# Kernel optimization log

Hardware: AMD Instinct MI355X
Metric: run time of the kernel (lower is better)

The kernel has to match this reference:

```python
import jax, jax.numpy as jnp
import numpy as np

# Structure constants (layered DAG form of the deepire proof trace)
M, D, R = 2, 128, 8          # ensemble size, embed dim, #inference rules
N0, L, K = 8192, 32, 4096    # init nodes, levels, deriv nodes per level
N_THAX, N_SINE = 1000, 32
N_TOTAL = N0 + L * K
POS_WEIGHT_EXTRA = 1.0


def setup_inputs() -> dict:
    key = jax.random.key(0)
    ks = jax.random.split(key, 8)
    rng = np.random.default_rng(0)
    # --- DAG structure (int, constant) ---
    thax_ids = jnp.asarray(rng.integers(0, N_THAX, N0), jnp.int32)
    sine_ids = jnp.asarray(rng.integers(0, N_SINE, N0), jnp.int32)
    # parents of level-l nodes come only from nodes created before level l
    parents = np.stack([rng.integers(0, N0 + l * K, (K, 2)) for l in range(L)])
    parents = jnp.asarray(parents.astype(np.int32))
    rule_ids = jnp.asarray(rng.integers(0, R, (L, K)), jnp.int32)
    sel = rng.random(N_TOTAL) < 0.1
    pos_cnt = jnp.asarray(np.where(sel, rng.integers(1, 20, N_TOTAL), 0), jnp.float32)
    neg_cnt = jnp.asarray(np.where(sel, rng.integers(0, 20, N_TOTAL), 0), jnp.float32)
    # --- learned params (per ensemble member) ---
    def p(k, shape, scale):
        return (scale * jax.random.normal(k, shape, jnp.float32))
    return dict(
        thax_ids=thax_ids, sine_ids=sine_ids, parents=parents, rule_ids=rule_ids,
        pos_cnt=pos_cnt, neg_cnt=neg_cnt,
        thax_table=p(ks[0], (M, N_THAX, D), 1.0),
        sine_w=p(ks[1], (M, D), 0.1),
        sine_b=p(ks[2], (M, D), 0.1),
        W1=p(ks[3], (M, R, 2 * D, D), (2 * D) ** -0.5),
        b1=jnp.zeros((M, R, D), jnp.float32),
        W2=p(ks[4], (M, R, D, D), D ** -0.5),
        b2=jnp.zeros((M, R, D), jnp.float32),
        w_eval=p(ks[5], (M, D), D ** -0.5),
        b_eval=jnp.zeros((M,), jnp.float32),
    )


def _forward(thax_ids, sine_ids, parents, rule_ids, pos_cnt, neg_cnt,
             thax_table, sine_w, sine_b, W1, b1, W2, b2, w_eval, b_eval):
    # --- init nodes: embedding lookup + sine embellishment ---
    emb = jnp.take(thax_table, thax_ids, axis=1)                  # [M, N0, D]
    s = sine_ids.astype(jnp.float32)[None, :, None]               # [1, N0, 1]
    emb = emb * jax.nn.sigmoid(s * sine_w[:, None, :] + sine_b[:, None, :])
    store = jnp.zeros((N_TOTAL, M, D), jnp.float32)
    store = store.at[:N0].set(jnp.transpose(emb, (1, 0, 2)))      # [N, M, D]

    offsets = N0 + K * jnp.arange(L, dtype=jnp.int32)

    def level(store, xs):
        par, rid, off = xs                                        # [K,2], [K], []
        pe = store[par]                                           # [K, 2, M, D]
        x = jnp.concatenate([pe[:, 0], pe[:, 1]], axis=-1)        # [K, M, 2D]
        # per-rule 2-layer MLP on concatenated parents (CatAndNonLinearBinary)
        h = jax.nn.relu(jnp.einsum('kmd,mrde->kmre', x, W1) + b1[None])
        h = jnp.einsum('kmre,mref->kmrf', h, W2) + b2[None]       # [K, M, R, D]
        new = jnp.take_along_axis(h, rid[:, None, None, None], axis=2)[:, :, 0]
        store = jax.lax.dynamic_update_slice(store, new, (off, 0, 0))
        return store, None

    store, _ = jax.lax.scan(level, store, (parents, rule_ids, offsets))

    # --- evaluation / loss on selected nodes ---
    vals = jnp.einsum('nmd,md->nm', store, w_eval) + b_eval       # [N, M] logits
    cnt = pos_cnt + neg_cnt
    mask = (cnt > 0).astype(jnp.float32)                          # [N]
    gold = jnp.where(cnt > 0, pos_cnt / jnp.maximum(cnt, 1.0), 0.0)
    tot_pos, tot_neg = jnp.sum(pos_cnt), jnp.sum(neg_cnt)
    pw = jnp.where(tot_pos > 0, POS_WEIGHT_EXTRA * tot_neg / jnp.maximum(tot_pos, 1.0), 1.0)
    # BCEWithLogits with pos_weight, stable form
    bce = pw * gold[:, None] * jax.nn.softplus(-vals) \
        + (1.0 - gold)[:, None] * jax.nn.softplus(vals)           # [N, M]
    loss = jnp.sum((mask * cnt)[:, None] * bce, axis=0)           # [M]
    posOK = jnp.sum(mask[:, None] * (vals >= 0) * pos_cnt[:, None], axis=0)
    negOK = jnp.sum(mask[:, None] * (vals < 0) * neg_cnt[:, None], axis=0)
    return loss, posOK, negOK


def reference(thax_ids, sine_ids, parents, rule_ids, pos_cnt, neg_cnt,
              thax_table, sine_w, sine_b, W1, b1, W2, b2, w_eval, b_eval):
    return _forward(thax_ids, sine_ids, parents, rule_ids, pos_cnt, neg_cnt,
                    thax_table, sine_w, sine_b, W1, b1, W2, b2, w_eval, b_eval)
```

## Files before the change

### kernel.cpp

```cpp
#include <hip/hip_runtime.h>
#include <cstdint>
#include <cstddef>

#define MM 2
#define DD 128
#define RR 8
#define NN0 8192
#define LLV 32
#define KK 4096
#define NTHAX 1000
#define NTOT (NN0 + LLV*KK)
#define NB 16
#define CHN16 264
#define EBLK 2048
#define TBLK 64

typedef short bf16x8 __attribute__((ext_vector_type(8)));
typedef float f32x4  __attribute__((ext_vector_type(4)));

__device__ __forceinline__ unsigned short f2bf(float f){
  union { float f; uint32_t u; } x; x.f = f;
  uint32_t u = x.u + 0x7FFFu + ((x.u >> 16) & 1u);
  return (unsigned short)(u >> 16);
}

__global__ void prep_kernel(const int* __restrict__ rule_ids,
                            int* __restrict__ chunk_nodes,
                            int* __restrict__ chunk_rule,
                            int* __restrict__ nchunks)
{
  const int l = blockIdx.x, t = threadIdx.x;
  __shared__ int cnt[RR], start[RR], fill[RR];
  if (t < RR){ cnt[t] = 0; fill[t] = 0; }
  __syncthreads();
  for (int k = t; k < KK; k += blockDim.x) atomicAdd(&cnt[rule_ids[l*KK + k]], 1);
  __syncthreads();
  if (t == 0){
    int s = 0;
    for (int r = 0; r < RR; ++r){
      start[r] = s;
      int pad = (cnt[r] + NB - 1)/NB*NB;
      for (int c = s/NB; c < (s+pad)/NB; ++c) chunk_rule[l*CHN16 + c] = r;
      s += pad;
    }
    nchunks[l] = s/NB;
  }
  __syncthreads();
  for (int i = t; i < CHN16*NB; i += blockDim.x) chunk_nodes[l*CHN16*NB + i] = -1;
  __syncthreads();
  for (int k = t; k < KK; k += blockDim.x){
    int r = rule_ids[l*KK + k];
    int p = start[r] + atomicAdd(&fill[r], 1);
    chunk_nodes[l*CHN16*NB + p] = k;
  }
}

__global__ void convw_kernel(const float* __restrict__ W, unsigned short* __restrict__ Wt, int K)
{
  int idx = blockIdx.x*blockDim.x + threadIdx.x;
  if (idx >= MM*RR*K*DD) return;
  int e = idx & 127;
  int k = (idx >> 7) % K;
  int mr = idx / (K*DD);
  float v = W[((size_t)mr*K + k)*DD + e];
  int kb = k >> 3, j = k & 7;
  Wt[((size_t)mr*(K >> 3) + kb)*DD*8 + e*8 + j] = f2bf(v);
}

__global__ void init_kernel(const int* __restrict__ thax_ids, const int* __restrict__ sine_ids,
                            const float* __restrict__ thax_table,
                            const float* __restrict__ sine_w, const float* __restrict__ sine_b,
                            float* __restrict__ store)
{
  int idx = blockIdx.x*blockDim.x + threadIdx.x;
  if (idx >= NN0*MM*DD) return;
  int i = idx >> 8;
  int md = idx & 255;
  int m = md >> 7, d = md & 127;
  float emb = thax_table[((size_t)m*NTHAX + thax_ids[i])*DD + d];
  float s = (float)sine_ids[i];
  float z = s*sine_w[m*DD + d] + sine_b[m*DD + d];
  float sig = 1.f/(1.f + expf(-z));
  store[idx] = emb*sig;
}

__global__ void totals_kernel(const float* __restrict__ pos, const float* __restrict__ neg,
                              float* __restrict__ pt)
{
  __shared__ float ts[4][2];
  const int t = threadIdx.x, lane = t & 63;
  float sp = 0.f, sn = 0.f;
  for (int n = blockIdx.x*blockDim.x + t; n < NTOT; n += gridDim.x*blockDim.x){
    sp += pos[n]; sn += neg[n];
  }
  #pragma unroll
  for (int s = 1; s < 64; s <<= 1){ sp += __shfl_xor(sp, s, 64); sn += __shfl_xor(sn, s, 64); }
  if (lane == 0){ ts[t>>6][0] = sp; ts[t>>6][1] = sn; }
  __syncthreads();
  if (t < 2) pt[t*TBLK + blockIdx.x] = ts[0][t] + ts[1][t] + ts[2][t] + ts[3][t];
}

__global__ __launch_bounds__(256, 2) void level_kernel(
    float* __restrict__ store,
    const int* __restrict__ parents,
    const int* __restrict__ chunk_nodes,
    const int* __restrict__ chunk_rule,
    const int* __restrict__ nchunks,
    const unsigned short* __restrict__ W1t, const float* __restrict__ b1,
    const unsigned short* __restrict__ W2t, const float* __restrict__ b2,
    int level)
{
  const int c = blockIdx.x;
  if (c >= nchunks[level]) return;
  const int m = blockIdx.y;
  const int r = chunk_rule[level*CHN16 + c];

  __shared__ __align__(16) unsigned short Xs[16*256];
  __shared__ __align__(16) unsigned short Hs[16*128];
  __shared__ int nd[NB];
  __shared__ int par[NB][2];

  const int t  = threadIdx.x;
  const int w  = t >> 6;
  const int l  = t & 63;
  const int lr = l & 15;
  const int lg = l >> 4;

  if (t < NB){
    int node = chunk_nodes[(level*CHN16 + c)*NB + t];
    nd[t] = node;
    const int* parL = parents + (size_t)level*KK*2;
    int p0 = 0, p1 = 0;
    if (node >= 0){ p0 = parL[node*2]; p1 = parL[node*2 + 1]; }
    par[t][0] = p0; par[t][1] = p1;
  }
  __syncthreads();

  #pragma unroll
  for (int q4 = 0; q4 < 4; ++q4){
    int q = q4*256 + t;
    int n = q >> 6, dq = q & 63;
    int p = par[n][dq >> 5];
    int col = (dq & 31)*4;
    float4 v = *(const float4*)(store + (size_t)p*(MM*DD) + m*DD + col);
    ushort4 b;
    b.x = f2bf(v.x); b.y = f2bf(v.y); b.z = f2bf(v.z); b.w = f2bf(v.w);
    int addr = n*512 + ((dq*8) ^ ((n & 7) << 4));
    *(ushort4*)((char*)Xs + addr) = b;
  }
  __syncthreads();

  const unsigned short* W1p = W1t + (size_t)(m*RR + r)*(256/8)*DD*8;
  f32x4 acc0 = {0.f,0.f,0.f,0.f}, acc1 = {0.f,0.f,0.f,0.f};
  #pragma unroll
  for (int s = 0; s < 8; ++s){
    int ab = lr*512 + ((s*64 + lg*16) ^ ((lr & 7) << 4));
    bf16x8 a = *(const bf16x8*)((const char*)Xs + ab);
    const unsigned short* bp = W1p + ((size_t)(s*4 + lg)*DD + w*32 + lr)*8;
    bf16x8 bf0 = *(const bf16x8*)bp;
    bf16x8 bf1 = *(const bf16x8*)(bp + 16*8);
    acc0 = __builtin_amdgcn_mfma_f32_16x16x32_bf16(a, bf0, acc0, 0, 0, 0);
    acc1 = __builtin_amdgcn_mfma_f32_16x16x32_bf16(a, bf1, acc1, 0, 0, 0);
  }

  {
    const float* b1v = b1 + (m*RR + r)*DD;
    int col0 = w*32 + lr;
    float bb0 = b1v[col0], bb1 = b1v[col0 + 16];
    #pragma unroll
    for (int reg = 0; reg < 4; ++reg){
      int row = lg*4 + reg;
      float h0 = fmaxf(acc0[reg] + bb0, 0.f);
      float h1 = fmaxf(acc1[reg] + bb1, 0.f);
      int sw = (row & 7) << 4;
      *(unsigned short*)((char*)Hs + row*256 + ((col0*2) ^ sw))        = f2bf(h0);
      *(unsigned short*)((char*)Hs + row*256 + (((col0 + 16)*2) ^ sw)) = f2bf(h1);
    }
  }
  __syncthreads();

  const unsigned short* W2p = W2t + (size_t)(m*RR + r)*(128/8)*DD*8;
  acc0 = (f32x4){0.f,0.f,0.f,0.f};
  acc1 = (f32x4){0.f,0.f,0.f,0.f};
  #pragma unroll
  for (int s = 0; s < 4; ++s){
    int ab = lr*256 + ((s*64 + lg*16) ^ ((lr & 7) << 4));
    bf16x8 a = *(const bf16x8*)((const char*)Hs + ab);
    const unsigned short* bp = W2p + ((size_t)(s*4 + lg)*DD + w*32 + lr)*8;
    bf16x8 bf0 = *(const bf16x8*)bp;
    bf16x8 bf1 = *(const bf16x8*)(bp + 16*8);
    acc0 = __builtin_amdgcn_mfma_f32_16x16x32_bf16(a, bf0, acc0, 0, 0, 0);
    acc1 = __builtin_amdgcn_mfma_f32_16x16x32_bf16(a, bf1, acc1, 0, 0, 0);
  }

  {
    const float* b2v = b2 + (m*RR + r)*DD;
    const size_t obase = (size_t)NN0 + (size_t)level*KK;
    int col0 = w*32 + lr;
    float bb0 = b2v[col0], bb1 = b2v[col0 + 16];
    #pragma unroll
    for (int reg = 0; reg < 4; ++reg){
      int row = lg*4 + reg;
      int node = nd[row];
      if (node >= 0){
        float* op = store + (obase + node)*(MM*DD) + m*DD;
        op[col0]      = acc0[reg] + bb0;
        op[col0 + 16] = acc1[reg] + bb1;
      }
    }
  }
}

__global__ void eval_kernel(const float* __restrict__ store,
                            const float* __restrict__ pos_cnt, const float* __restrict__ neg_cnt,
                            const float* __restrict__ w_eval, const float* __restrict__ b_eval,
                            float* __restrict__ pe)
{
  __shared__ float part[4][2][4];
  const int t = threadIdx.x, lane = t & 63;
  const int gw = blockIdx.x*(blockDim.x >> 6) + (t >> 6);
  const int nw = gridDim.x*(blockDim.x >> 6);
  float4 wv = *(const float4*)&w_eval[4*lane];
  const int m = (lane >= 32) ? 1 : 0;
  const float be = b_eval[m];
  float A = 0.f, B = 0.f, pOK = 0.f, nOK = 0.f;
  for (int n = gw; n < NTOT; n += nw){
    float4 v = *(const float4*)&store[(size_t)n*(MM*DD) + 4*lane];
    float p = v.x*wv.x + v.y*wv.y + v.z*wv.z + v.w*wv.w;
    #pragma unroll
    for (int s = 1; s < 32; s <<= 1) p += __shfl_xor(p, s, 64);
    const float val = p + be;
    if ((lane & 31) == 0){
      const float pc = pos_cnt[n], nc = neg_cnt[n];
      const float cnt = pc + nc;
      if (cnt > 0.f){
        float gold = pc / fmaxf(cnt, 1.f);
        float e = log1pf(expf(-fabsf(val)));
        float sp_pos = e + fmaxf(val, 0.f);
        float sp_neg = e + fmaxf(-val, 0.f);
        A += cnt * gold * sp_neg;
        B += cnt * (1.f - gold) * sp_pos;
      }
      pOK += (val >= 0.f) ? pc : 0.f;
      nOK += (val <  0.f) ? nc : 0.f;
    }
  }
  if ((lane & 31) == 0){
    int wv2 = t >> 6;
    part[wv2][m][0] = A; part[wv2][m][1] = B; part[wv2][m][2] = pOK; part[wv2][m][3] = nOK;
  }
  __syncthreads();
  if (t < 8){
    int q = t >> 1, mm = t & 1;
    float s = part[0][mm][q] + part[1][mm][q] + part[2][mm][q] + part[3][mm][q];
    pe[t*EBLK + blockIdx.x] = s;
  }
}

__global__ void finish_kernel(const float* __restrict__ pt, const float* __restrict__ pe,
                              float* __restrict__ out)
{
  __shared__ float acc8[8];
  __shared__ float tt[2];
  const int t = threadIdx.x;
  if (t < 64){
    int c = t >> 5, l = t & 31;
    float s = pt[c*TBLK + l] + pt[c*TBLK + l + 32];
    #pragma unroll
    for (int d = 1; d < 32; d <<= 1) s += __shfl_xor(s, d, 64);
    if (l == 0) tt[c] = s;
  }
  {
    int comp = t >> 5, l = t & 31;
    float s = 0.f;
    for (int i = 0; i < EBLK/32; ++i) s += pe[comp*EBLK + i*32 + l];
    #pragma unroll
    for (int d = 1; d < 32; d <<= 1) s += __shfl_xor(s, d, 64);
    if (l == 0) acc8[comp] = s;
  }
  __syncthreads();
  if (t < 2){
    float tp = tt[0], tn = tt[1];
    float pw = (tp > 0.f) ? (tn / fmaxf(tp, 1.f)) : 1.f;
    out[t]     = pw*acc8[0 + t] + acc8[2 + t];
    out[2 + t] = acc8[4 + t];
    out[4 + t] = acc8[6 + t];
  }
}

extern "C" void kernel_launch(void* const* d_in, const int* in_sizes, int n_in,
                              void* d_out, int out_size, void* d_ws, size_t ws_size,
                              hipStream_t stream)
{
  const int*   thax_ids   = (const int*)d_in[0];
  const int*   sine_ids   = (const int*)d_in[1];
  const int*   parents    = (const int*)d_in[2];
  const int*   rule_ids   = (const int*)d_in[3];
  const float* pos_cnt    = (const float*)d_in[4];
  const float* neg_cnt    = (const float*)d_in[5];
  const float* thax_table = (const float*)d_in[6];
  const float* sine_w     = (const float*)d_in[7];
  const float* sine_b     = (const float*)d_in[8];
  const float* W1         = (const float*)d_in[9];
  const float* b1         = (const float*)d_in[10];
  const float* W2         = (const float*)d_in[11];
  const float* b2         = (const float*)d_in[12];
  const float* w_eval     = (const float*)d_in[13];
  const float* b_eval     = (const float*)d_in[14];

  char* ws = (char*)d_ws;
  float* store = (float*)ws;
  size_t off = (size_t)NTOT*MM*DD*sizeof(float);
  int* chunk_nodes = (int*)(ws + off); off += (size_t)LLV*CHN16*NB*sizeof(int);
  int* chunk_rule  = (int*)(ws + off); off += (size_t)LLV*CHN16*sizeof(int);
  int* nchunks     = (int*)(ws + off); off += (size_t)LLV*sizeof(int);
  float* pt        = (float*)(ws + off); off += (size_t)2*TBLK*sizeof(float);
  float* pe        = (float*)(ws + off); off += (size_t)8*EBLK*sizeof(float);
  off = (off + 15) & ~(size_t)15;
  unsigned short* W1t = (unsigned short*)(ws + off); off += (size_t)MM*RR*256*DD*sizeof(unsigned short);
  unsigned short* W2t = (unsigned short*)(ws + off); off += (size_t)MM*RR*128*DD*sizeof(unsigned short);

  prep_kernel<<<LLV, 256, 0, stream>>>(rule_ids, chunk_nodes, chunk_rule, nchunks);
  convw_kernel<<<(MM*RR*256*DD + 255)/256, 256, 0, stream>>>(W1, W1t, 256);
  convw_kernel<<<(MM*RR*128*DD + 255)/256, 256, 0, stream>>>(W2, W2t, 128);
  init_kernel<<<(NN0*MM*DD + 255)/256, 256, 0, stream>>>(thax_ids, sine_ids, thax_table,
                                                         sine_w, sine_b, store);
  totals_kernel<<<TBLK, 256, 0, stream>>>(pos_cnt, neg_cnt, pt);

  for (int l = 0; l < LLV; ++l)
    level_kernel<<<dim3(CHN16, MM), 256, 0, stream>>>(store, parents, chunk_nodes, chunk_rule,
                                                      nchunks, W1t, b1, W2t, b2, l);

  eval_kernel<<<EBLK, 256, 0, stream>>>(store, pos_cnt, neg_cnt, w_eval, b_eval, pe);
  finish_kernel<<<1, 256, 0, stream>>>(pt, pe, (float*)d_out);
}
```

Baseline: 352.3 us.

## Store node embeddings as bf16 and remap level-kernel blocks for weight locality

```diff
diff --git a/kernel.cpp b/kernel.cpp
--- a/kernel.cpp
+++ b/kernel.cpp
@@ -23,6 +23,9 @@
   uint32_t u = x.u + 0x7FFFu + ((x.u >> 16) & 1u);
   return (unsigned short)(u >> 16);
 }
+__device__ __forceinline__ float bf2f(unsigned short h){
+  union { uint32_t u; float f; } x; x.u = ((uint32_t)h) << 16; return x.f;
+}
 
 __global__ void prep_kernel(const int* __restrict__ rule_ids,
                             int* __restrict__ chunk_nodes,
@@ -55,22 +58,33 @@
   }
 }
 
-__global__ void convw_kernel(const float* __restrict__ W, unsigned short* __restrict__ Wt, int K)
+__global__ void convw_kernel(const float* __restrict__ W1, const float* __restrict__ W2,
+                             unsigned short* __restrict__ W1t, unsigned short* __restrict__ W2t)
 {
   int idx = blockIdx.x*blockDim.x + threadIdx.x;
-  if (idx >= MM*RR*K*DD) return;
-  int e = idx & 127;
-  int k = (idx >> 7) % K;
-  int mr = idx / (K*DD);
-  float v = W[((size_t)mr*K + k)*DD + e];
-  int kb = k >> 3, j = k & 7;
-  Wt[((size_t)mr*(K >> 3) + kb)*DD*8 + e*8 + j] = f2bf(v);
+  const int N1 = MM*RR*256*DD;
+  const int N2 = MM*RR*128*DD;
+  if (idx < N1){
+    int e = idx & 127;
+    int k = (idx >> 7) & 255;
+    int mr = idx >> 15;
+    float v = W1[((size_t)mr*256 + k)*DD + e];
+    W1t[((size_t)mr*32 + (k >> 3))*DD*8 + e*8 + (k & 7)] = f2bf(v);
+  } else {
+    idx -= N1;
+    if (idx >= N2) return;
+    int e = idx & 127;
+    int k = (idx >> 7) & 127;
+    int mr = idx >> 14;
+    float v = W2[((size_t)mr*128 + k)*DD + e];
+    W2t[((size_t)mr*16 + (k >> 3))*DD*8 + e*8 + (k & 7)] = f2bf(v);
+  }
 }
 
 __global__ void init_kernel(const int* __restrict__ thax_ids, const int* __restrict__ sine_ids,
                             const float* __restrict__ thax_table,
                             const float* __restrict__ sine_w, const float* __restrict__ sine_b,
-                            float* __restrict__ store)
+                            unsigned short* __restrict__ store)
 {
   int idx = blockIdx.x*blockDim.x + threadIdx.x;
   if (idx >= NN0*MM*DD) return;
@@ -81,7 +95,7 @@
   float s = (float)sine_ids[i];
   float z = s*sine_w[m*DD + d] + sine_b[m*DD + d];
   float sig = 1.f/(1.f + expf(-z));
-  store[idx] = emb*sig;
+  store[idx] = f2bf(emb*sig);
 }
 
 __global__ void totals_kernel(const float* __restrict__ pos, const float* __restrict__ neg,
@@ -100,8 +114,8 @@
   if (t < 2) pt[t*TBLK + blockIdx.x] = ts[0][t] + ts[1][t] + ts[2][t] + ts[3][t];
 }
 
-__global__ __launch_bounds__(256, 2) void level_kernel(
-    float* __restrict__ store,
+__global__ __launch_bounds__(256, 4) void level_kernel(
+    unsigned short* __restrict__ store,
     const int* __restrict__ parents,
     const int* __restrict__ chunk_nodes,
     const int* __restrict__ chunk_rule,
@@ -110,9 +124,10 @@
     const unsigned short* __restrict__ W2t, const float* __restrict__ b2,
     int level)
 {
-  const int c = blockIdx.x;
+  const int bid = blockIdx.x;
+  const int c = (bid >> 4)*8 + (bid & 7);
+  const int m = (bid >> 3) & 1;
   if (c >= nchunks[level]) return;
-  const int m = blockIdx.y;
   const int r = chunk_rule[level*CHN16 + c];
 
   __shared__ __align__(16) unsigned short Xs[16*256];
@@ -142,11 +157,9 @@
     int n = q >> 6, dq = q & 63;
     int p = par[n][dq >> 5];
     int col = (dq & 31)*4;
-    float4 v = *(const float4*)(store + (size_t)p*(MM*DD) + m*DD + col);
-    ushort4 b;
-    b.x = f2bf(v.x); b.y = f2bf(v.y); b.z = f2bf(v.z); b.w = f2bf(v.w);
+    ushort4 v = *(const ushort4*)(store + (size_t)p*(MM*DD) + m*DD + col);
     int addr = n*512 + ((dq*8) ^ ((n & 7) << 4));
-    *(ushort4*)((char*)Xs + addr) = b;
+    *(ushort4*)((char*)Xs + addr) = v;
   }
   __syncthreads();
 
@@ -203,15 +216,15 @@
       int row = lg*4 + reg;
       int node = nd[row];
       if (node >= 0){
-        float* op = store + (obase + node)*(MM*DD) + m*DD;
-        op[col0]      = acc0[reg] + bb0;
-        op[col0 + 16] = acc1[reg] + bb1;
+        unsigned short* op = store + (obase + node)*(MM*DD) + m*DD;
+        op[col0]      = f2bf(acc0[reg] + bb0);
+        op[col0 + 16] = f2bf(acc1[reg] + bb1);
       }
     }
   }
 }
 
-__global__ void eval_kernel(const float* __restrict__ store,
+__global__ void eval_kernel(const unsigned short* __restrict__ store,
                             const float* __restrict__ pos_cnt, const float* __restrict__ neg_cnt,
                             const float* __restrict__ w_eval, const float* __restrict__ b_eval,
                             float* __restrict__ pe)
@@ -225,8 +238,8 @@
   const float be = b_eval[m];
   float A = 0.f, B = 0.f, pOK = 0.f, nOK = 0.f;
   for (int n = gw; n < NTOT; n += nw){
-    float4 v = *(const float4*)&store[(size_t)n*(MM*DD) + 4*lane];
-    float p = v.x*wv.x + v.y*wv.y + v.z*wv.z + v.w*wv.w;
+    ushort4 v4 = *(const ushort4*)&store[(size_t)n*(MM*DD) + 4*lane];
+    float p = bf2f(v4.x)*wv.x + bf2f(v4.y)*wv.y + bf2f(v4.z)*wv.z + bf2f(v4.w)*wv.w;
     #pragma unroll
     for (int s = 1; s < 32; s <<= 1) p += __shfl_xor(p, s, 64);
     const float val = p + be;
@@ -309,8 +322,9 @@
   const float* b_eval     = (const float*)d_in[14];
 
   char* ws = (char*)d_ws;
-  float* store = (float*)ws;
-  size_t off = (size_t)NTOT*MM*DD*sizeof(float);
+  unsigned short* store = (unsigned short*)ws;
+  size_t off = (size_t)NTOT*MM*DD*sizeof(unsigned short);
+  off = (off + 15) & ~(size_t)15;
   int* chunk_nodes = (int*)(ws + off); off += (size_t)LLV*CHN16*NB*sizeof(int);
   int* chunk_rule  = (int*)(ws + off); off += (size_t)LLV*CHN16*sizeof(int);
   int* nchunks     = (int*)(ws + off); off += (size_t)LLV*sizeof(int);
@@ -321,15 +335,14 @@
   unsigned short* W2t = (unsigned short*)(ws + off); off += (size_t)MM*RR*128*DD*sizeof(unsigned short);
 
   prep_kernel<<<LLV, 256, 0, stream>>>(rule_ids, chunk_nodes, chunk_rule, nchunks);
-  convw_kernel<<<(MM*RR*256*DD + 255)/256, 256, 0, stream>>>(W1, W1t, 256);
-  convw_kernel<<<(MM*RR*128*DD + 255)/256, 256, 0, stream>>>(W2, W2t, 128);
+  convw_kernel<<<(MM*RR*(256+128)*DD + 255)/256, 256, 0, stream>>>(W1, W2, W1t, W2t);
   init_kernel<<<(NN0*MM*DD + 255)/256, 256, 0, stream>>>(thax_ids, sine_ids, thax_table,
                                                          sine_w, sine_b, store);
   totals_kernel<<<TBLK, 256, 0, stream>>>(pos_cnt, neg_cnt, pt);
 
   for (int l = 0; l < LLV; ++l)
-    level_kernel<<<dim3(CHN16, MM), 256, 0, stream>>>(store, parents, chunk_nodes, chunk_rule,
-                                                      nchunks, W1t, b1, W2t, b2, l);
+    level_kernel<<<CHN16*2, 256, 0, stream>>>(store, parents, chunk_nodes, chunk_rule,
+                                              nchunks, W1t, b1, W2t, b2, l);
 
   eval_kernel<<<EBLK, 256, 0, stream>>>(store, pos_cnt, neg_cnt, w_eval, b_eval, pe);
   finish_kernel<<<1, 256, 0, stream>>>(pt, pe, (float*)d_out);
```

Result: faster. 328.5 us (-6.7%).
